# Performance work log

Hardware: AMD Instinct MI355X
Metric: run time of the kernel (lower is better)

The kernel has to match this reference:

```python
import jax, jax.numpy as jnp
import numpy as np

EMBED = 768
HEAD = 64

def setup_inputs() -> dict:
    key = jax.random.key(0)
    k1, k2, k3, k4 = jax.random.split(key, 4)
    x = jax.random.normal(k1, (8, 2048, EMBED), dtype=jnp.float32)
    # torch nn.Linear weights: [out, in], applied as x @ W.T
    scale = 1.0 / np.sqrt(EMBED)
    Wq = jax.random.uniform(k2, (HEAD, EMBED), jnp.float32, -scale, scale)
    Wk = jax.random.uniform(k3, (HEAD, EMBED), jnp.float32, -scale, scale)
    Wv = jax.random.uniform(k4, (HEAD, EMBED), jnp.float32, -scale, scale)
    return {"x": x, "Wq": Wq, "Wk": Wk, "Wv": Wv}

def reference(x, Wq, Wk, Wv):
    B, S, E = x.shape
    q = jnp.einsum('bse,he->bsh', x, Wq)
    k = jnp.einsum('bse,he->bsh', x, Wk)
    v = jnp.einsum('bse,he->bsh', x, Wv)
    # NOTE: faithful to source: weights / embed**(-0.5) == weights * sqrt(embed)
    scores = jnp.einsum('bqh,bkh->bqk', q, k) * jnp.sqrt(jnp.float32(E))
    causal = jnp.tril(jnp.ones((S, S), dtype=bool))
    scores = jnp.where(causal, scores, -jnp.inf)
    attn = jax.nn.softmax(scores, axis=-1)
    return jnp.einsum('bqk,bkh->bqh', attn, v)
```

## Files before the change

### kernel.cpp

```cpp
#include <hip/hip_runtime.h>
#include <math.h>

#define EMBED 768
#define SEQ   2048
#define NB    8
#define QSCALE 39.98113776623437f

typedef short  short8 __attribute__((ext_vector_type(8)));
typedef float  f32x4  __attribute__((ext_vector_type(4)));
typedef float  f32x16 __attribute__((ext_vector_type(16)));

#define WHI_OFF  0u
#define WLO_OFF  147456u
#define QHI_OFF  294912u
#define QLO_OFF  (294912u + 1u*1048576u)
#define KHI_OFF  (294912u + 2u*1048576u)
#define KLO_OFF  (294912u + 3u*1048576u)
#define VT_OFF   (294912u + 4u*1048576u)
#define FLT_BASE 2768896u

__device__ __forceinline__ ushort f2bf(float f) {
    unsigned u = __float_as_uint(f);
    return (ushort)((u + 0x7FFFu + ((u >> 16) & 1u)) >> 16);
}
__device__ __forceinline__ ushort f2bf_trunc(float f) {
    return (ushort)(__float_as_uint(f) >> 16);
}
__device__ __forceinline__ float bf2f(ushort h) {
    return __uint_as_float(((unsigned)h) << 16);
}
__device__ __forceinline__ uint cvtpk(float a, float b) {
    uint r;
    asm("v_cvt_pk_bf16_f32 %0, %1, %2" : "=v"(r) : "v"(a), "v"(b));
    return r;
}

union U8 { uint u[4]; short8 s; };

__global__ __launch_bounds__(256)
void split_w_kernel(const float* __restrict__ Wq, const float* __restrict__ Wk,
                    const float* __restrict__ Wv,
                    ushort* __restrict__ w_hi, ushort* __restrict__ w_lo)
{
    int idx = blockIdx.x * 256 + threadIdx.x;
    if (idx >= 192 * EMBED) return;
    int row = idx / EMBED, e = idx - row * EMBED;
    float f;
    if (row < 64)       f = Wq[row * EMBED + e] * QSCALE;
    else if (row < 128) f = Wk[(row - 64) * EMBED + e];
    else                f = Wv[(row - 128) * EMBED + e];
    ushort hi = f2bf(f);
    w_hi[idx] = hi;
    w_lo[idx] = f2bf_trunc(f - bf2f(hi));
}

__global__ __launch_bounds__(256)
void proj_kernel(const float* __restrict__ x,
                 const ushort* __restrict__ w_hi, const ushort* __restrict__ w_lo,
                 ushort* __restrict__ q_hi, ushort* __restrict__ q_lo,
                 ushort* __restrict__ k_hi, ushort* __restrict__ k_lo,
                 ushort* __restrict__ v_t)
{
    __shared__ __align__(16) ushort xa_hi[32][72], xa_lo[32][72];
    __shared__ __align__(16) ushort wbh[192][72];
    __shared__ __align__(16) ushort wbl[128][72];

    const int t    = threadIdx.x;
    const int lane = t & 63;
    const int wid  = t >> 6;
    const int ln   = lane & 15;
    const int kg   = lane >> 4;
    const int row0 = blockIdx.x * 32;

    const int srow = t >> 3;
    const int scol = (t & 7) * 8;
    const int wrow = t >> 2;
    const int wcol = (t & 3) * 16;

    float4 xr0, xr1;
    short8 wh0, wh1, wh2, wh3, wh4, wh5;
    short8 wl0, wl1, wl2, wl3;

#define LOAD_CHUNK(e0) do {                                                     \
        const float*  xp_ = x + (size_t)(row0 + srow) * EMBED + (e0) + scol;    \
        xr0 = *(const float4*)xp_;  xr1 = *(const float4*)(xp_ + 4);            \
        const ushort* whp_ = w_hi + (size_t)wrow * EMBED + (e0) + wcol;         \
        wh0 = *(const short8*)whp_;                                             \
        wh1 = *(const short8*)(whp_ + 8);                                       \
        wh2 = *(const short8*)(whp_ + 64 * EMBED);                              \
        wh3 = *(const short8*)(whp_ + 64 * EMBED + 8);                          \
        wh4 = *(const short8*)(whp_ + 128 * EMBED);                             \
        wh5 = *(const short8*)(whp_ + 128 * EMBED + 8);                         \
        const ushort* wlp_ = w_lo + (size_t)wrow * EMBED + (e0) + wcol;         \
        wl0 = *(const short8*)wlp_;                                             \
        wl1 = *(const short8*)(wlp_ + 8);                                       \
        wl2 = *(const short8*)(wlp_ + 64 * EMBED);                              \
        wl3 = *(const short8*)(wlp_ + 64 * EMBED + 8);                          \
    } while (0)

    const f32x4 vzero = {0.f, 0.f, 0.f, 0.f};
    f32x4 acc[2][3];
#pragma unroll
    for (int mt = 0; mt < 2; ++mt)
#pragma unroll
        for (int j = 0; j < 3; ++j) acc[mt][j] = vzero;

    LOAD_CHUNK(0);

    for (int c = 0; c < 12; ++c) {
        if (c) __syncthreads();
        {
            const float fv[8] = {xr0.x, xr0.y, xr0.z, xr0.w,
                                 xr1.x, xr1.y, xr1.z, xr1.w};
            short8 h0, l0;
#pragma unroll
            for (int i = 0; i < 8; ++i) {
                ushort h = f2bf(fv[i]);
                h0[i] = (short)h;
                l0[i] = (short)f2bf_trunc(fv[i] - bf2f(h));
            }
            *(short8*)&xa_hi[srow][scol] = h0;
            *(short8*)&xa_lo[srow][scol] = l0;
            *(short8*)&wbh[wrow][wcol]           = wh0;
            *(short8*)&wbh[wrow][wcol + 8]       = wh1;
            *(short8*)&wbh[wrow + 64][wcol]      = wh2;
            *(short8*)&wbh[wrow + 64][wcol + 8]  = wh3;
            *(short8*)&wbh[wrow + 128][wcol]     = wh4;
            *(short8*)&wbh[wrow + 128][wcol + 8] = wh5;
            *(short8*)&wbl[wrow][wcol]           = wl0;
            *(short8*)&wbl[wrow][wcol + 8]       = wl1;
            *(short8*)&wbl[wrow + 64][wcol]      = wl2;
            *(short8*)&wbl[wrow + 64][wcol + 8]  = wl3;
        }
        __syncthreads();
        if (c < 11) LOAD_CHUNK((c + 1) * 64);

        short8 ah[2][2], al[2][2];
#pragma unroll
        for (int mt = 0; mt < 2; ++mt)
#pragma unroll
            for (int ks = 0; ks < 2; ++ks) {
                ah[mt][ks] = *(const short8*)&xa_hi[mt * 16 + ln][ks * 32 + kg * 8];
                al[mt][ks] = *(const short8*)&xa_lo[mt * 16 + ln][ks * 32 + kg * 8];
            }
#pragma unroll
        for (int j = 0; j < 3; ++j) {
            const int ntg = j * 4 + wid;
#pragma unroll
            for (int ks = 0; ks < 2; ++ks) {
                const int co = ks * 32 + kg * 8;
                if (j < 2) {
                    short8 bh = *(const short8*)&wbh[ntg * 16 + ln][co];
                    short8 bl = *(const short8*)&wbl[ntg * 16 + ln][co];
#pragma unroll
                    for (int mt = 0; mt < 2; ++mt) {
                        acc[mt][j] = __builtin_amdgcn_mfma_f32_16x16x32_bf16(ah[mt][ks], bh, acc[mt][j], 0, 0, 0);
                        acc[mt][j] = __builtin_amdgcn_mfma_f32_16x16x32_bf16(ah[mt][ks], bl, acc[mt][j], 0, 0, 0);
                        acc[mt][j] = __builtin_amdgcn_mfma_f32_16x16x32_bf16(al[mt][ks], bh, acc[mt][j], 0, 0, 0);
                    }
                } else {
                    short8 bh = *(const short8*)&wbh[ntg * 16 + ln][co];
#pragma unroll
                    for (int mt = 0; mt < 2; ++mt)
                        acc[mt][j] = __builtin_amdgcn_mfma_f32_16x16x32_bf16(ah[mt][ks], bh, acc[mt][j], 0, 0, 0);
                }
            }
        }
    }
#undef LOAD_CHUNK

#pragma unroll
    for (int mt = 0; mt < 2; ++mt) {
        const int rbase = row0 + mt * 16 + kg * 4;
#pragma unroll
        for (int j = 0; j < 3; ++j) {
            const int col = (j * 4 + wid) * 16 + ln;
#pragma unroll
            for (int r = 0; r < 4; ++r) {
                int rg = rbase + r;
                int b = rg >> 11, s = rg & 2047;
                size_t rowoff = ((size_t)b * SEQ + s) * 64;
                float val = acc[mt][j][r];
                if (col < 64) {
                    ushort h = f2bf(val);
                    q_hi[rowoff + col] = h;
                    q_lo[rowoff + col] = f2bf_trunc(val - bf2f(h));
                } else if (col < 128) {
                    ushort h = f2bf(val);
                    k_hi[rowoff + (col - 64)] = h;
                    k_lo[rowoff + (col - 64)] = f2bf_trunc(val - bf2f(h));
                } else {
                    v_t[((size_t)b * 64 + (col - 128)) * SEQ + s] = f2bf(val);
                }
            }
        }
    }
}

__global__ __launch_bounds__(256)
void attn_kernel(const ushort* __restrict__ q_hi, const ushort* __restrict__ q_lo,
                 const ushort* __restrict__ k_hi, const ushort* __restrict__ k_lo,
                 const ushort* __restrict__ v_t,
                 float* __restrict__ oP, float* __restrict__ mP,
                 float* __restrict__ lP, int Z)
{
    __shared__ __align__(16) ushort kv[2][3][64][64];

    const int t    = threadIdx.x;
    const int lane = t & 63;
    const int w    = t >> 6;
    const int l31  = lane & 31;
    const int h8   = (lane >> 5) << 3;
    const int sw   = (lane & 7) << 3;
    const int b    = blockIdx.x & 7;
    const int pr   = (blockIdx.x >> 3) & 7;
    const int z    = blockIdx.x >> 6;
    const int qA   = 15 - pr;
    const int qB   = pr;
    const int cA   = 2 * qA + 2;
    const int T    = cA + 2 * qB + 2;

    const ushort* qhb = q_hi + (size_t)b * SEQ * 64;
    const ushort* qlb = q_lo + (size_t)b * SEQ * 64;
    const ushort* khb = k_hi + (size_t)b * SEQ * 64;
    const ushort* klb = k_lo + (size_t)b * SEQ * 64;
    const ushort* vtb = v_t + (size_t)b * 64 * SEQ;
    float* oPz = oP + (size_t)z * 1048576u;
    float* mPz = mP + (size_t)z * 16384u;
    float* lPz = lP + (size_t)z * 16384u;

    const int srow8 = lane >> 3;
    const int scol  = ((lane & 7) << 3) ^ ((lane >> 3) << 3);

    auto stage = [&](int g, int cbuf) {
        const int kk = (g < cA) ? g : g - cA;
        const int j0 = kk << 6;
        ushort* base = &kv[cbuf][0][0][0];
#pragma unroll
        for (int s = 0; s < 6; ++s) {
            const int i = w * 6 + s;
            const int row = ((i & 7) << 3) + srow8;
            const ushort* gp;
            if (i < 8)       gp = khb + (size_t)(j0 + row) * 64 + scol;
            else if (i < 16) gp = klb + (size_t)(j0 + row) * 64 + scol;
            else             gp = vtb + (size_t)row * SEQ + j0 + scol;
            __builtin_amdgcn_global_load_lds(
                (const __attribute__((address_space(1))) void*)gp,
                (__attribute__((address_space(3))) void*)(base + i * 512),
                16, 0, 0);
        }
    };

    auto loadQ = [&](int qb, short8 (&qh)[4], short8 (&ql)[4]) {
#pragma unroll
        for (int ks = 0; ks < 4; ++ks) {
            size_t off = (size_t)(qb * 128 + w * 32 + l31) * 64 + ks * 16 + h8;
            qh[ks] = *(const short8*)(qhb + off);
            ql[ks] = *(const short8*)(qlb + off);
        }
    };

    auto body = [&](int kk, int qb, f32x16 (&o)[2], float& m_run, float& l_run,
                    short8 (&qh)[4], short8 (&ql)[4], int cbuf) {
        const ushort* K0 = &kv[cbuf][0][0][0];
        const ushort* K1 = &kv[cbuf][1][0][0];
        const ushort* VT = &kv[cbuf][2][0][0];

        f32x16 sacc[2];
#pragma unroll
        for (int i = 0; i < 16; ++i) { sacc[0][i] = 0.f; sacc[1][i] = 0.f; }
#pragma unroll
        for (int kt = 0; kt < 2; ++kt) {
            const int rb = (kt * 32 + l31) * 64;
#pragma unroll
            for (int ks = 0; ks < 4; ++ks) {
                const int c = (ks * 16 + h8) ^ sw;
                short8 ah = *(const short8*)(K0 + rb + c);
                short8 al = *(const short8*)(K1 + rb + c);
                sacc[kt] = __builtin_amdgcn_mfma_f32_32x32x16_bf16(ah, qh[ks], sacc[kt], 0, 0, 0);
                sacc[kt] = __builtin_amdgcn_mfma_f32_32x32x16_bf16(ah, ql[ks], sacc[kt], 0, 0, 0);
                sacc[kt] = __builtin_amdgcn_mfma_f32_32x32x16_bf16(al, qh[ks], sacc[kt], 0, 0, 0);
            }
        }

        if ((kk >> 1) == qb) {
            const int q   = qb * 128 + w * 32 + l31;
            const int hi4 = (lane >> 5) << 2;
#pragma unroll
            for (int kt = 0; kt < 2; ++kt) {
                const int kb = kk * 64 + kt * 32 + hi4;
#pragma unroll
                for (int reg = 0; reg < 16; ++reg) {
                    const int key = kb + (reg & 3) + 8 * (reg >> 2);
                    if (key > q) sacc[kt][reg] = -1e30f;
                }
            }
        }

        float t8[8];
#pragma unroll
        for (int j = 0; j < 8; ++j)
            t8[j] = fmaxf(fmaxf(sacc[0][2*j], sacc[0][2*j+1]),
                          fmaxf(sacc[1][2*j], sacc[1][2*j+1]));
        float mx = fmaxf(fmaxf(fmaxf(t8[0], t8[1]), fmaxf(t8[2], t8[3])),
                         fmaxf(fmaxf(t8[4], t8[5]), fmaxf(t8[6], t8[7])));
        mx = fmaxf(mx, __shfl_xor(mx, 32));
        float mn   = fmaxf(m_run, mx);
        float corr = exp2f(m_run - mn);
        float p[2][16];
        float lt = 0.f;
#pragma unroll
        for (int kt = 0; kt < 2; ++kt)
#pragma unroll
            for (int reg = 0; reg < 16; ++reg) {
                p[kt][reg] = exp2f(sacc[kt][reg] - mn);
                lt += p[kt][reg];
            }
        lt += __shfl_xor(lt, 32);
        m_run = mn;
        l_run = l_run * corr + lt;
        o[0] = o[0] * corr;
        o[1] = o[1] * corr;

        const bool hiH = (lane >= 32);
#pragma unroll
        for (int kt = 0; kt < 2; ++kt) {
            uint pk[8], rx[8];
#pragma unroll
            for (int j = 0; j < 8; ++j) pk[j] = cvtpk(p[kt][2*j], p[kt][2*j+1]);
#pragma unroll
            for (int j = 0; j < 8; ++j) rx[j] = (uint)__shfl_xor((int)pk[j], 32);
            U8 f0, f1;
            f0.u[0] = hiH ? rx[2] : pk[0];
            f0.u[1] = hiH ? rx[3] : pk[1];
            f0.u[2] = hiH ? pk[2] : rx[0];
            f0.u[3] = hiH ? pk[3] : rx[1];
            f1.u[0] = hiH ? rx[6] : pk[4];
            f1.u[1] = hiH ? rx[7] : pk[5];
            f1.u[2] = hiH ? pk[6] : rx[4];
            f1.u[3] = hiH ? pk[7] : rx[5];
#pragma unroll
            for (int ht = 0; ht < 2; ++ht) {
                const int row = ht * 32 + l31;
#pragma unroll
                for (int s2 = 0; s2 < 2; ++s2) {
                    const int c = (kt * 32 + s2 * 16 + h8) ^ sw;
                    short8 av = *(const short8*)(VT + row * 64 + c);
                    o[ht] = __builtin_amdgcn_mfma_f32_32x32x16_bf16(
                                av, (s2 ? f1.s : f0.s), o[ht], 0, 0, 0);
                }
            }
        }
    };

    auto storeP = [&](int qb, f32x16 (&o)[2], float m_run, float l_run) {
        const size_t rowq = (size_t)b * SEQ + qb * 128 + w * 32 + l31;
        const int hb = (lane >> 5) << 2;
        float* op = oPz + rowq * 64;
#pragma unroll
        for (int ht = 0; ht < 2; ++ht)
#pragma unroll
            for (int rq = 0; rq < 4; ++rq) {
                float4 v = make_float4(o[ht][4*rq], o[ht][4*rq+1],
                                       o[ht][4*rq+2], o[ht][4*rq+3]);
                *(float4*)(op + ht * 32 + rq * 8 + hb) = v;
            }
        if (lane < 32) { mPz[rowq] = m_run; lPz[rowq] = l_run; }
    };

    short8 qh[4], ql[4];
    f32x16 o[2];
    float m_run, l_run;

    int g = z;
    stage(g, 0);
    loadQ(qA, qh, ql);
#pragma unroll
    for (int i = 0; i < 16; ++i) { o[0][i] = 0.f; o[1][i] = 0.f; }
    m_run = -INFINITY; l_run = 0.f;
    __syncthreads();
    int cur = 0;

    while (g < cA) {
        const int gn = g + Z;
        if (gn < T) stage(gn, cur ^ 1);
        body(g, qA, o, m_run, l_run, qh, ql, cur);
        __syncthreads();
        cur ^= 1; g = gn;
    }
    storeP(qA, o, m_run, l_run);

    loadQ(qB, qh, ql);
#pragma unroll
    for (int i = 0; i < 16; ++i) { o[0][i] = 0.f; o[1][i] = 0.f; }
    m_run = -INFINITY; l_run = 0.f;

    while (g < T) {
        const int gn = g + Z;
        if (gn < T) stage(gn, cur ^ 1);
        body(g - cA, qB, o, m_run, l_run, qh, ql, cur);
        __syncthreads();
        cur ^= 1; g = gn;
    }
    storeP(qB, o, m_run, l_run);
}

__global__ __launch_bounds__(256)
void merge_kernel(const float* __restrict__ oP, const float* __restrict__ mP,
                  const float* __restrict__ lP, float* __restrict__ out, int Z)
{
    int idx = blockIdx.x * 256 + threadIdx.x;
    int R  = idx >> 4;
    int h0 = (idx & 15) << 2;
    float M = -INFINITY;
    for (int zz = 0; zz < Z; ++zz) M = fmaxf(M, mP[zz * 16384 + R]);
    float L = 0.f;
    float4 acc = make_float4(0.f, 0.f, 0.f, 0.f);
    for (int zz = 0; zz < Z; ++zz) {
        float c = exp2f(mP[zz * 16384 + R] - M);
        L += lP[zz * 16384 + R] * c;
        float4 a = *(const float4*)(oP + (size_t)zz * 1048576u + (size_t)R * 64 + h0);
        acc.x += a.x * c; acc.y += a.y * c; acc.z += a.z * c; acc.w += a.w * c;
    }
    float inv = 1.0f / L;
    float4 r = make_float4(acc.x * inv, acc.y * inv, acc.z * inv, acc.w * inv);
    *(float4*)(out + (size_t)R * 64 + h0) = r;
}

extern "C" void kernel_launch(void* const* d_in, const int* in_sizes, int n_in,
                              void* d_out, int out_size, void* d_ws, size_t ws_size,
                              hipStream_t stream)
{
    const float* x  = (const float*)d_in[0];
    const float* Wq = (const float*)d_in[1];
    const float* Wk = (const float*)d_in[2];
    const float* Wv = (const float*)d_in[3];
    float* out = (float*)d_out;

    ushort* ws = (ushort*)d_ws;
    float*  wsf = (float*)d_ws;
    ushort* w_hi = ws + WHI_OFF;
    ushort* w_lo = ws + WLO_OFF;
    ushort* q_hi = ws + QHI_OFF;
    ushort* q_lo = ws + QLO_OFF;
    ushort* k_hi = ws + KHI_OFF;
    ushort* k_lo = ws + KLO_OFF;
    ushort* v_t  = ws + VT_OFF;

    int Z = 8;
    {
        size_t need8 = ((size_t)FLT_BASE + 8u * (1048576u + 32768u)) * 4u;
        if (ws_size < need8) Z = 4;
    }
    float* oP = wsf + FLT_BASE;
    float* mP = oP + (size_t)Z * 1048576u;
    float* lP = mP + (size_t)Z * 16384u;

    split_w_kernel<<<dim3(576), dim3(256), 0, stream>>>(Wq, Wk, Wv, w_hi, w_lo);
    proj_kernel<<<dim3(512), dim3(256), 0, stream>>>(x, w_hi, w_lo,
                                                     q_hi, q_lo, k_hi, k_lo, v_t);
    attn_kernel<<<dim3(64 * Z), dim3(256), 0, stream>>>(q_hi, q_lo, k_hi, k_lo, v_t,
                                                        oP, mP, lP, Z);
    merge_kernel<<<dim3(1024), dim3(256), 0, stream>>>(oP, mP, lP, out, Z);
}
```

Measured before the change: 62.42 us.

## Triple-buffer K/V staging with single barrier loop, setprio around MFMAs, permlane32 swap

The attention kernel moves from a double-buffered to a triple-buffered LDS ring and prefetches two tiles ahead. Each iteration uses one explicit vmcnt wait plus a barrier instead of a trailing __syncthreads, and the two query-block loops are merged into one loop that switches to the second block in place. MFMA sections are wrapped in s_setprio to favour matrix issue, and the 32-lane P exchange uses permlane32_swap instead of shfl_xor plus selects. Together these aim to hide global-load latency and cut cross-lane shuffle cost. The cost is 50% more LDS, which may lower occupancy, and a hard-coded vmcnt that depends on the load count in stage.

```diff
diff --git a/kernel.cpp b/kernel.cpp
--- a/kernel.cpp
+++ b/kernel.cpp
@@ -9,6 +9,7 @@
 typedef short  short8 __attribute__((ext_vector_type(8)));
 typedef float  f32x4  __attribute__((ext_vector_type(4)));
 typedef float  f32x16 __attribute__((ext_vector_type(16)));
+typedef unsigned int uint2v __attribute__((ext_vector_type(2)));
 
 #define WHI_OFF  0u
 #define WLO_OFF  147456u
@@ -204,7 +205,7 @@
                  float* __restrict__ oP, float* __restrict__ mP,
                  float* __restrict__ lP, int Z)
 {
-    __shared__ __align__(16) ushort kv[2][3][64][64];
+    __shared__ __align__(16) ushort kv[3][3][64][64];
 
     const int t    = threadIdx.x;
     const int lane = t & 63;
@@ -218,7 +219,7 @@
     const int qA   = 15 - pr;
     const int qB   = pr;
     const int cA   = 2 * qA + 2;
-    const int T    = cA + 2 * qB + 2;
+    const int T    = 34;
 
     const ushort* qhb = q_hi + (size_t)b * SEQ * 64;
     const ushort* qlb = q_lo + (size_t)b * SEQ * 64;
@@ -269,6 +270,7 @@
         f32x16 sacc[2];
 #pragma unroll
         for (int i = 0; i < 16; ++i) { sacc[0][i] = 0.f; sacc[1][i] = 0.f; }
+        __builtin_amdgcn_s_setprio(1);
 #pragma unroll
         for (int kt = 0; kt < 2; ++kt) {
             const int rb = (kt * 32 + l31) * 64;
@@ -282,6 +284,7 @@
                 sacc[kt] = __builtin_amdgcn_mfma_f32_32x32x16_bf16(al, qh[ks], sacc[kt], 0, 0, 0);
             }
         }
+        __builtin_amdgcn_s_setprio(0);
 
         if ((kk >> 1) == qb) {
             const int q   = qb * 128 + w * 32 + l31;
@@ -322,15 +325,24 @@
         o[0] = o[0] * corr;
         o[1] = o[1] * corr;
 
-        const bool hiH = (lane >= 32);
 #pragma unroll
         for (int kt = 0; kt < 2; ++kt) {
-            uint pk[8], rx[8];
+            uint pk[8];
 #pragma unroll
             for (int j = 0; j < 8; ++j) pk[j] = cvtpk(p[kt][2*j], p[kt][2*j+1]);
+            U8 f0, f1;
+#if __has_builtin(__builtin_amdgcn_permlane32_swap)
+            uint2v a0 = __builtin_amdgcn_permlane32_swap(pk[0], pk[2], false, false);
+            uint2v b0 = __builtin_amdgcn_permlane32_swap(pk[1], pk[3], false, false);
+            uint2v a1 = __builtin_amdgcn_permlane32_swap(pk[4], pk[6], false, false);
+            uint2v b1 = __builtin_amdgcn_permlane32_swap(pk[5], pk[7], false, false);
+            f0.u[0] = a0.x; f0.u[1] = b0.x; f0.u[2] = a0.y; f0.u[3] = b0.y;
+            f1.u[0] = a1.x; f1.u[1] = b1.x; f1.u[2] = a1.y; f1.u[3] = b1.y;
+#else
+            const bool hiH = (lane >= 32);
+            uint rx[8];
 #pragma unroll
             for (int j = 0; j < 8; ++j) rx[j] = (uint)__shfl_xor((int)pk[j], 32);
-            U8 f0, f1;
             f0.u[0] = hiH ? rx[2] : pk[0];
             f0.u[1] = hiH ? rx[3] : pk[1];
             f0.u[2] = hiH ? pk[2] : rx[0];
@@ -339,6 +351,8 @@
             f1.u[1] = hiH ? rx[7] : pk[5];
             f1.u[2] = hiH ? pk[6] : rx[4];
             f1.u[3] = hiH ? pk[7] : rx[5];
+#endif
+            __builtin_amdgcn_s_setprio(1);
 #pragma unroll
             for (int ht = 0; ht < 2; ++ht) {
                 const int row = ht * 32 + l31;
@@ -350,6 +364,7 @@
                                 av, (s2 ? f1.s : f0.s), o[ht], 0, 0, 0);
                 }
             }
+            __builtin_amdgcn_s_setprio(0);
         }
     };
 
@@ -372,37 +387,46 @@
     f32x16 o[2];
     float m_run, l_run;
 
-    int g = z;
-    stage(g, 0);
+    const int cnt = (T - 1 - z) / Z + 1;
+    stage(z, 0);
+    stage(z + Z, 1);
     loadQ(qA, qh, ql);
 #pragma unroll
     for (int i = 0; i < 16; ++i) { o[0][i] = 0.f; o[1][i] = 0.f; }
     m_run = -INFINITY; l_run = 0.f;
-    __syncthreads();
-    int cur = 0;
-
-    while (g < cA) {
-        const int gn = g + Z;
-        if (gn < T) stage(gn, cur ^ 1);
-        body(g, qA, o, m_run, l_run, qh, ql, cur);
-        __syncthreads();
-        cur ^= 1; g = gn;
-    }
-    storeP(qA, o, m_run, l_run);
-
-    loadQ(qB, qh, ql);
-#pragma unroll
-    for (int i = 0; i < 16; ++i) { o[0][i] = 0.f; o[1][i] = 0.f; }
-    m_run = -INFINITY; l_run = 0.f;
-
-    while (g < T) {
-        const int gn = g + Z;
-        if (gn < T) stage(gn, cur ^ 1);
-        body(g - cA, qB, o, m_run, l_run, qh, ql, cur);
-        __syncthreads();
-        cur ^= 1; g = gn;
-    }
-    storeP(qB, o, m_run, l_run);
+    bool inB = false;
+
+    for (int i = 0; i < cnt; ++i) {
+        const int g = z + i * Z;
+        asm volatile("s_waitcnt vmcnt(6)" ::: "memory");
+        __builtin_amdgcn_s_barrier();
+        if (i + 2 < cnt) stage(z + (i + 2) * Z, (i + 2) % 3);
+        if (g >= cA && !inB) {
+            storeP(qA, o, m_run, l_run);
+            loadQ(qB, qh, ql);
+#pragma unroll
+            for (int j = 0; j < 16; ++j) { o[0][j] = 0.f; o[1][j] = 0.f; }
+            m_run = -INFINITY; l_run = 0.f;
+            inB = true;
+        }
+        body(g < cA ? g : g - cA, g < cA ? qA : qB, o, m_run, l_run, qh, ql, i % 3);
+    }
+
+    if (!inB) {
+        storeP(qA, o, m_run, l_run);
+        const size_t rowq = (size_t)b * SEQ + qB * 128 + w * 32 + l31;
+        float* op = oPz + rowq * 64;
+        const int hb = (lane >> 5) << 2;
+        float4 zz = make_float4(0.f, 0.f, 0.f, 0.f);
+#pragma unroll
+        for (int ht = 0; ht < 2; ++ht)
+#pragma unroll
+            for (int rq = 0; rq < 4; ++rq)
+                *(float4*)(op + ht * 32 + rq * 8 + hb) = zz;
+        if (lane < 32) { mPz[rowq] = -INFINITY; lPz[rowq] = 0.f; }
+    } else {
+        storeP(qB, o, m_run, l_run);
+    }
 }
 
 __global__ __launch_bounds__(256)
```

New measurement: 61.37 us. About the same (-1.7%).
